# Kernel optimization log

Measured on AMD Instinct MI355X. Metric: run time of the kernel, lower is better.

Reference implementation:

```python
import jax, jax.numpy as jnp
import numpy as np

HIDDEN = 1024
N_HEADS = 16
HEAD_DIM = HIDDEN // N_HEADS
WINDOW = 256
HALF_W = WINDOW // 2  # 128
GLOBAL_TOKENS = (0,)


def setup_inputs() -> dict:
    key = jax.random.key(0)
    ks = jax.random.split(key, 5)
    B, S = 1, 4096
    scale = 0.02
    return {
        "x": jax.random.normal(ks[0], (B, S, HIDDEN), dtype=jnp.float32),
        "Wq": jax.random.normal(ks[1], (HIDDEN, HIDDEN), dtype=jnp.float32) * scale,
        "Wk": jax.random.normal(ks[2], (HIDDEN, HIDDEN), dtype=jnp.float32) * scale,
        "Wv": jax.random.normal(ks[3], (HIDDEN, HIDDEN), dtype=jnp.float32) * scale,
        "Wo": jax.random.normal(ks[4], (HIDDEN, HIDDEN), dtype=jnp.float32) * scale,
    }


def _longformer_mask(seq_len: int) -> jnp.ndarray:
    # sliding window |i-j| <= half_w, plus full rows/cols for global tokens
    idx = jnp.arange(seq_len)
    mask = jnp.abs(idx[:, None] - idx[None, :]) <= HALF_W
    for g in GLOBAL_TOKENS:
        if 0 <= g < seq_len:
            mask = mask.at[g, :].set(True)
            mask = mask.at[:, g].set(True)
    return mask  # [S, S] bool


def reference(x, Wq, Wk, Wv, Wo):
    B, S, H = x.shape
    scale = HEAD_DIM ** -0.5
    # nn.Linear(bias=False): y = x @ W.T ; split heads -> [B, nH, S, hd]
    def proj(W):
        return jnp.einsum('bsh,oh->bso', x, W).reshape(B, S, N_HEADS, HEAD_DIM).transpose(0, 2, 1, 3)
    q, k, v = proj(Wq), proj(Wk), proj(Wv)
    scores = jnp.einsum('bnsd,bntd->bnst', q, k) * scale  # [B, nH, S, S]
    mask = _longformer_mask(S)
    scores = jnp.where(mask[None, None], scores, jnp.float32(-jnp.inf))
    attn = jax.nn.softmax(scores, axis=-1)
    out = jnp.einsum('bnst,bntd->bnsd', attn, v)  # [B, nH, S, hd]
    out = out.transpose(0, 2, 1, 3).reshape(B, S, H)
    return jnp.einsum('bsh,oh->bso', out, Wo)
```

## Files before the change

### kernel.cpp

```cpp
#include <hip/hip_runtime.h>
#include <hip/hip_bf16.h>
#include <stdint.h>

#define S_LEN 4096
#define HID   1024
#define NH    16
#define HD    64
#define HWIN  128

typedef __bf16 bf16x8 __attribute__((ext_vector_type(8)));
typedef float  f32x4  __attribute__((ext_vector_type(4)));
typedef unsigned short u16x8 __attribute__((ext_vector_type(8)));

typedef const __attribute__((address_space(1))) unsigned int* gas_ptr;
typedef __attribute__((address_space(3))) unsigned int* las_ptr;

__device__ __forceinline__ float bf2f(unsigned short u) {
  union { float f; uint32_t i; } w; w.i = ((uint32_t)u) << 16; return w.f;
}
__device__ __forceinline__ unsigned short f2bf(float f) {
  union { float f; uint32_t i; } w; w.f = f;
  uint32_t r = (w.i + 0x7FFFu + ((w.i >> 16) & 1u)) >> 16;
  return (unsigned short)r;
}

__device__ __forceinline__ void gld_lds16(const void* g, void* l) {
  __builtin_amdgcn_global_load_lds((gas_ptr)g, (las_ptr)l, 16, 0, 0);
}

__global__ __launch_bounds__(256) void convert_all(
    const float* __restrict__ x,
    const float* __restrict__ wq, const float* __restrict__ wk,
    const float* __restrict__ wv, const float* __restrict__ wo,
    unsigned short* __restrict__ xb,
    unsigned short* __restrict__ wqb, unsigned short* __restrict__ wkb,
    unsigned short* __restrict__ wvb, unsigned short* __restrict__ wob) {
  const float* in; unsigned short* out; int n4;
  switch (blockIdx.y) {
    case 0:  in = x;  out = xb;  n4 = (S_LEN * HID) / 4; break;
    case 1:  in = wq; out = wqb; n4 = (HID * HID) / 4;   break;
    case 2:  in = wk; out = wkb; n4 = (HID * HID) / 4;   break;
    case 3:  in = wv; out = wvb; n4 = (HID * HID) / 4;   break;
    default: in = wo; out = wob; n4 = (HID * HID) / 4;   break;
  }
  int i = blockIdx.x * 256 + threadIdx.x;
  if (i >= n4) return;
  float4 v = reinterpret_cast<const float4*>(in)[i];
  ushort4 o;
  o.x = f2bf(v.x); o.y = f2bf(v.y); o.z = f2bf(v.z); o.w = f2bf(v.w);
  reinterpret_cast<ushort4*>(out)[i] = o;
}

__device__ __forceinline__ void gemm_body(const unsigned short* __restrict__ A,
                                          const unsigned short* __restrict__ B,
                                          unsigned short* __restrict__ Cb,
                                          float* __restrict__ Cf, int mode) {
  __shared__ __align__(16) unsigned short As[128 * 64];
  __shared__ __align__(16) unsigned short Bs[128 * 64];
  constexpr int K = HID;
  const int tid  = threadIdx.x;
  const int lane = tid & 63;
  const int wave = tid >> 6;
  const int wm = wave >> 1, wn = wave & 1;
  const int m0 = blockIdx.x * 128;
  const int n0 = blockIdx.y * 128;
  const int cl = lane & 15, g = lane >> 4;

  f32x4 acc[4][4];
#pragma unroll
  for (int i = 0; i < 4; i++)
#pragma unroll
    for (int j = 0; j < 4; j++) acc[i][j] = f32x4{0.f, 0.f, 0.f, 0.f};

  const unsigned short* Ap[4];
  const unsigned short* Bp[4];
  int ldso[4];
#pragma unroll
  for (int u = 0; u < 4; u++) {
    int s = tid + u * 256;
    int row = s >> 3, c16 = s & 7;
    int sc = ((c16 ^ (row & 7)) << 3);
    Ap[u] = A + (size_t)(m0 + row) * K + sc;
    Bp[u] = B + (size_t)(n0 + row) * K + sc;
    ldso[u] = s * 8;
  }

  for (int k0 = 0; k0 < K; k0 += 64) {
#pragma unroll
    for (int u = 0; u < 4; u++) {
      gld_lds16(Ap[u] + k0, &As[ldso[u]]);
      gld_lds16(Bp[u] + k0, &Bs[ldso[u]]);
    }
    __syncthreads();
#pragma unroll
    for (int kk = 0; kk < 2; kk++) {
      bf16x8 a[4], b[4];
#pragma unroll
      for (int mi = 0; mi < 4; mi++) {
        int row = wm * 64 + mi * 16 + cl;
        int c16 = (kk * 4 + g) ^ (row & 7);
        a[mi] = *reinterpret_cast<const bf16x8*>(&As[row * 64 + c16 * 8]);
      }
#pragma unroll
      for (int ni = 0; ni < 4; ni++) {
        int row = wn * 64 + ni * 16 + cl;
        int c16 = (kk * 4 + g) ^ (row & 7);
        b[ni] = *reinterpret_cast<const bf16x8*>(&Bs[row * 64 + c16 * 8]);
      }
#pragma unroll
      for (int mi = 0; mi < 4; mi++)
#pragma unroll
        for (int ni = 0; ni < 4; ni++)
          acc[mi][ni] = __builtin_amdgcn_mfma_f32_16x16x32_bf16(a[mi], b[ni], acc[mi][ni], 0, 0, 0);
    }
    __syncthreads();
  }

  const int rl = g * 4;
#pragma unroll
  for (int mi = 0; mi < 4; mi++)
#pragma unroll
    for (int ni = 0; ni < 4; ni++)
#pragma unroll
      for (int i = 0; i < 4; i++) {
        int r = m0 + wm * 64 + mi * 16 + rl + i;
        int c = n0 + wn * 64 + ni * 16 + cl;
        float v = acc[mi][ni][i];
        if (mode == 2)      Cf[(size_t)r * HID + c] = v;
        else if (mode == 1) Cb[(size_t)c * S_LEN + r] = f2bf(v);
        else                Cb[(size_t)r * HID + c] = f2bf(v);
      }
}

__global__ __launch_bounds__(256, 2) void gemm_qkv(
    const unsigned short* __restrict__ xb,
    const unsigned short* __restrict__ wqb, const unsigned short* __restrict__ wkb,
    const unsigned short* __restrict__ wvb,
    unsigned short* __restrict__ Qb, unsigned short* __restrict__ Kb,
    unsigned short* __restrict__ Vt) {
  const unsigned short* B = (blockIdx.z == 0) ? wqb : (blockIdx.z == 1) ? wkb : wvb;
  unsigned short* C       = (blockIdx.z == 0) ? Qb  : (blockIdx.z == 1) ? Kb  : Vt;
  int mode = (blockIdx.z == 2) ? 1 : 0;
  gemm_body(xb, B, C, nullptr, mode);
}

__global__ __launch_bounds__(256, 2) void gemm_proj(
    const unsigned short* __restrict__ Ob, const unsigned short* __restrict__ wob,
    float* __restrict__ out) {
  gemm_body(Ob, wob, nullptr, out, 2);
}

__global__ __launch_bounds__(256) void attn_win(
    const unsigned short* __restrict__ Qb,
    const unsigned short* __restrict__ Kb,
    const unsigned short* __restrict__ Vt,
    unsigned short* __restrict__ Ob) {
  __shared__ __align__(16) unsigned short Kl[2][64 * 64];
  __shared__ __align__(16) unsigned short Vl[2][64 * 64];
  __shared__ __align__(16) unsigned short Ps[4][16 * 64];
  const int L  = (blockIdx.x & 7) * 128 + (blockIdx.x >> 3);
  const int h  = L >> 6;
  const int q0 = (L & 63) * 64;
  const int tid  = threadIdx.x;
  const int lane = tid & 63;
  const int wave = tid >> 6;
  const int qr   = q0 + wave * 16;
  const int cl = lane & 15, g = lane >> 4, rl = g * 4;
  const float SCL = 0.125f * 1.44269504f;

  int kw0 = q0 - 128; if (kw0 < 0) kw0 = 0;
  int kw1 = q0 + 192; if (kw1 > S_LEN) kw1 = S_LEN;
  const int nc = (kw1 - kw0) >> 6;

  const int s0 = tid, s1 = tid + 256;
  const int kr0 = s0 >> 3, kc0 = ((s0 & 7) ^ (kr0 & 7)) << 3;
  const int kr1 = s1 >> 3, kc1 = ((s1 & 7) ^ (kr1 & 7)) << 3;
  const unsigned short* Kbase = Kb + h * HD;
  const unsigned short* Vbase = Vt + (size_t)h * HD * S_LEN;

  auto stage = [&](int kb, int b) {
    gld_lds16(Kbase + (size_t)(kb + kr0) * HID + kc0, &Kl[b][s0 * 8]);
    gld_lds16(Kbase + (size_t)(kb + kr1) * HID + kc1, &Kl[b][s1 * 8]);
    gld_lds16(Vbase + (size_t)kr0 * S_LEN + kb + kc0, &Vl[b][s0 * 8]);
    gld_lds16(Vbase + (size_t)kr1 * S_LEN + kb + kc1, &Vl[b][s1 * 8]);
  };

  stage(kw0, 0);

  bf16x8 qf[2], k0f[2];
  {
    const unsigned short* qb = Qb + (size_t)(qr + cl) * HID + h * HD + g * 8;
    qf[0] = *reinterpret_cast<const bf16x8*>(qb);
    qf[1] = *reinterpret_cast<const bf16x8*>(qb + 32);
    const unsigned short* k0 = Kb + h * HD + g * 8;
    k0f[0] = *reinterpret_cast<const bf16x8*>(k0);
    k0f[1] = *reinterpret_cast<const bf16x8*>(k0 + 32);
  }
  float v0[4];
#pragma unroll
  for (int nt = 0; nt < 4; nt++)
    v0[nt] = bf2f(Vt[(size_t)(h * HD + nt * 16 + cl) * S_LEN]);

  float m_i[4] = {-1e30f, -1e30f, -1e30f, -1e30f};
  float l_i[4] = {0.f, 0.f, 0.f, 0.f};
  f32x4 oacc[4];
#pragma unroll
  for (int nt = 0; nt < 4; nt++) oacc[nt] = f32x4{0.f, 0.f, 0.f, 0.f};

  __syncthreads();

  for (int c = 0; c < nc; c++) {
    const int cur = c & 1;
    const int kb = kw0 + c * 64;
    if (c + 1 < nc) stage(kw0 + (c + 1) * 64, cur ^ 1);

    bf16x8 kf[4][2];
#pragma unroll
    for (int t = 0; t < 4; t++) {
      int R = t * 16 + cl;
      kf[t][0] = *reinterpret_cast<const bf16x8*>(&Kl[cur][R * 64 + ((g ^ (R & 7)) << 3)]);
      kf[t][1] = *reinterpret_cast<const bf16x8*>(&Kl[cur][R * 64 + (((g + 4) ^ (R & 7)) << 3)]);
    }
    f32x4 s4[4];
#pragma unroll
    for (int t = 0; t < 4; t++) {
      s4[t] = f32x4{0.f, 0.f, 0.f, 0.f};
      s4[t] = __builtin_amdgcn_mfma_f32_16x16x32_bf16(qf[0], kf[t][0], s4[t], 0, 0, 0);
      s4[t] = __builtin_amdgcn_mfma_f32_16x16x32_bf16(qf[1], kf[t][1], s4[t], 0, 0, 0);
    }
    float sv[4][4], tm[4];
    if (kb >= qr - 113 && kb <= qr + 65) {
#pragma unroll
      for (int i = 0; i < 4; i++) {
        tm[i] = -1e30f;
#pragma unroll
        for (int t = 0; t < 4; t++) {
          float v = s4[t][i] * SCL;
          sv[t][i] = v;
          tm[i] = fmaxf(tm[i], v);
        }
      }
    } else {
#pragma unroll
      for (int i = 0; i < 4; i++) {
        int row = qr + rl + i;
        tm[i] = -1e30f;
#pragma unroll
        for (int t = 0; t < 4; t++) {
          int col = kb + t * 16 + cl;
          int d = row - col;
          float v = (d <= HWIN && d >= -HWIN) ? s4[t][i] * SCL : -1e30f;
          sv[t][i] = v;
          tm[i] = fmaxf(tm[i], v);
        }
      }
    }
#pragma unroll
    for (int dd = 1; dd < 16; dd <<= 1)
#pragma unroll
      for (int i = 0; i < 4; i++) tm[i] = fmaxf(tm[i], __shfl_xor(tm[i], dd, 16));

    float p[4][4], ps[4];
#pragma unroll
    for (int i = 0; i < 4; i++) {
      float mnew = fmaxf(m_i[i], tm[i]);
      float fac  = exp2f(m_i[i] - mnew);
      m_i[i] = mnew;
      float sum = 0.f;
#pragma unroll
      for (int t = 0; t < 4; t++) { p[t][i] = exp2f(sv[t][i] - mnew); sum += p[t][i]; }
      ps[i] = sum;
      l_i[i] *= fac;
#pragma unroll
      for (int nt = 0; nt < 4; nt++) oacc[nt][i] *= fac;
    }
#pragma unroll
    for (int dd = 1; dd < 16; dd <<= 1)
#pragma unroll
      for (int i = 0; i < 4; i++) ps[i] += __shfl_xor(ps[i], dd, 16);
#pragma unroll
    for (int i = 0; i < 4; i++) l_i[i] += ps[i];

#pragma unroll
    for (int t = 0; t < 4; t++)
#pragma unroll
      for (int i = 0; i < 4; i++) {
        int row = rl + i;
        Ps[wave][row * 64 + ((t * 16 + cl) ^ ((row & 7) << 3))] = f2bf(p[t][i]);
      }
    bf16x8 pf[2];
    pf[0] = *reinterpret_cast<const bf16x8*>(&Ps[wave][cl * 64 + ((g * 8) ^ ((cl & 7) << 3))]);
    pf[1] = *reinterpret_cast<const bf16x8*>(&Ps[wave][cl * 64 + ((32 + g * 8) ^ ((cl & 7) << 3))]);

#pragma unroll
    for (int nt = 0; nt < 4; nt++) {
      int row = nt * 16 + cl;
      bf16x8 vf0 = *reinterpret_cast<const bf16x8*>(&Vl[cur][row * 64 + ((g ^ (row & 7)) << 3)]);
      bf16x8 vf1 = *reinterpret_cast<const bf16x8*>(&Vl[cur][row * 64 + (((g + 4) ^ (row & 7)) << 3)]);
      oacc[nt] = __builtin_amdgcn_mfma_f32_16x16x32_bf16(pf[0], vf0, oacc[nt], 0, 0, 0);
      oacc[nt] = __builtin_amdgcn_mfma_f32_16x16x32_bf16(pf[1], vf1, oacc[nt], 0, 0, 0);
    }

    __syncthreads();
  }

  float part = 0.f;
#pragma unroll
  for (int s = 0; s < 2; s++)
#pragma unroll
    for (int j = 0; j < 8; j++) part += (float)qf[s][j] * (float)k0f[s][j];
  part += __shfl_xor(part, 16);
  part += __shfl_xor(part, 32);
  float s0q = part * SCL;
#pragma unroll
  for (int i = 0; i < 4; i++) {
    float z0 = __shfl(s0q, rl + i, 16);
    int row = qr + rl + i;
    if (row > HWIN) {
      float mnew = fmaxf(m_i[i], z0);
      float fac  = exp2f(m_i[i] - mnew);
      float p0   = exp2f(z0 - mnew);
      l_i[i] = l_i[i] * fac + p0;
#pragma unroll
      for (int nt = 0; nt < 4; nt++)
        oacc[nt][i] = oacc[nt][i] * fac + p0 * v0[nt];
    }
  }

#pragma unroll
  for (int nt = 0; nt < 4; nt++)
#pragma unroll
    for (int i = 0; i < 4; i++)
      Ob[(size_t)(qr + rl + i) * HID + h * HD + nt * 16 + cl] = f2bf(oacc[nt][i] / l_i[i]);
}

__global__ __launch_bounds__(256) void attn_row0_part(
    const unsigned short* __restrict__ Qb,
    const unsigned short* __restrict__ Kb,
    const unsigned short* __restrict__ Vt,
    float* __restrict__ mw, float* __restrict__ lw, float* __restrict__ ow) {
  const int h = blockIdx.y, c = blockIdx.x;
  const int tid = threadIdx.x, lane = tid & 63, wave = tid >> 6;
  const int k = c * 256 + tid;
  __shared__ float qsh[HD];
  __shared__ float ps[256];
  __shared__ float redm[4], redl[4];
  __shared__ float red2[4][HD];
  const float LOG2E = 1.44269504f;

  if (tid < HD) qsh[tid] = bf2f(Qb[h * HD + tid]);
  __syncthreads();

  const unsigned short* kr = Kb + (size_t)k * HID + h * HD;
  float acc = 0.f;
#pragma unroll
  for (int v8 = 0; v8 < 8; v8++) {
    u16x8 kv = *reinterpret_cast<const u16x8*>(kr + v8 * 8);
#pragma unroll
    for (int j = 0; j < 8; j++) acc += qsh[v8 * 8 + j] * bf2f(kv[j]);
  }
  float s = acc * 0.125f;

  float m = s;
#pragma unroll
  for (int d = 1; d < 64; d <<= 1) m = fmaxf(m, __shfl_xor(m, d, 64));
  if (lane == 0) redm[wave] = m;
  __syncthreads();
  float m_c = fmaxf(fmaxf(redm[0], redm[1]), fmaxf(redm[2], redm[3]));

  float p = exp2f((s - m_c) * LOG2E);
  ps[tid] = p;
  float l = p;
#pragma unroll
  for (int d = 1; d < 64; d <<= 1) l += __shfl_xor(l, d, 64);
  if (lane == 0) redl[wave] = l;
  __syncthreads();
  float l_c = redl[0] + redl[1] + redl[2] + redl[3];

  const int d = tid & 63, grp = tid >> 6;
  const unsigned short* vrow = Vt + (size_t)(h * HD + d) * S_LEN + c * 256 + grp * 64;
  float a2 = 0.f;
#pragma unroll
  for (int v8 = 0; v8 < 8; v8++) {
    u16x8 vv = *reinterpret_cast<const u16x8*>(vrow + v8 * 8);
#pragma unroll
    for (int j = 0; j < 8; j++) a2 += ps[grp * 64 + v8 * 8 + j] * bf2f(vv[j]);
  }
  red2[grp][d] = a2;
  __syncthreads();
  if (tid < HD) {
    float o = red2[0][tid] + red2[1][tid] + red2[2][tid] + red2[3][tid];
    ow[(size_t)(h * 16 + c) * HD + tid] = o;
  }
  if (tid == 0) { mw[h * 16 + c] = m_c; lw[h * 16 + c] = l_c; }
}

__global__ __launch_bounds__(64) void attn_row0_fin(
    const float* __restrict__ mw, const float* __restrict__ lw,
    const float* __restrict__ ow, unsigned short* __restrict__ Ob) {
  const int h = blockIdx.x, d = threadIdx.x;
  const float LOG2E = 1.44269504f;
  float m_g = -1e30f;
#pragma unroll
  for (int c = 0; c < 16; c++) m_g = fmaxf(m_g, mw[h * 16 + c]);
  float lsum = 0.f, osum = 0.f;
#pragma unroll
  for (int c = 0; c < 16; c++) {
    float w = exp2f((mw[h * 16 + c] - m_g) * LOG2E);
    lsum += lw[h * 16 + c] * w;
    osum += ow[(size_t)(h * 16 + c) * HD + d] * w;
  }
  Ob[h * HD + d] = f2bf(osum / lsum);
}

extern "C" void kernel_launch(void* const* d_in, const int* in_sizes, int n_in,
                              void* d_out, int out_size, void* d_ws, size_t ws_size,
                              hipStream_t stream) {
  const float* x  = (const float*)d_in[0];
  const float* wq = (const float*)d_in[1];
  const float* wk = (const float*)d_in[2];
  const float* wv = (const float*)d_in[3];
  const float* wo = (const float*)d_in[4];
  float* out = (float*)d_out;
  char* ws = (char*)d_ws;
  const size_t MB = 1024ull * 1024ull;
  unsigned short* xb  = (unsigned short*)(ws + 0 * MB);
  unsigned short* wqb = (unsigned short*)(ws + 8 * MB);
  unsigned short* wkb = (unsigned short*)(ws + 10 * MB);
  unsigned short* wvb = (unsigned short*)(ws + 12 * MB);
  unsigned short* wob = (unsigned short*)(ws + 14 * MB);
  unsigned short* Qb  = (unsigned short*)(ws + 16 * MB);
  unsigned short* Kb  = (unsigned short*)(ws + 24 * MB);
  unsigned short* Vt  = (unsigned short*)(ws + 32 * MB);
  unsigned short* Ob  = (unsigned short*)(ws + 40 * MB);
  float* mw = (float*)(ws + 48 * MB);
  float* lw = (float*)(ws + 48 * MB + 4096);
  float* ow = (float*)(ws + 48 * MB + 8192);

  dim3 blk(256);
  convert_all<<<dim3((S_LEN * HID / 4 + 255) / 256, 5), blk, 0, stream>>>(
      x, wq, wk, wv, wo, xb, wqb, wkb, wvb, wob);
  gemm_qkv<<<dim3(S_LEN / 128, HID / 128, 3), blk, 0, stream>>>(
      xb, wqb, wkb, wvb, Qb, Kb, Vt);
  attn_win<<<dim3(1024), blk, 0, stream>>>(Qb, Kb, Vt, Ob);
  attn_row0_part<<<dim3(16, NH), blk, 0, stream>>>(Qb, Kb, Vt, mw, lw, ow);
  attn_row0_fin<<<dim3(NH), dim3(64), 0, stream>>>(mw, lw, ow, Ob);
  gemm_proj<<<dim3(S_LEN / 128, HID / 128), blk, 0, stream>>>(Ob, wob, out);
}
```

Baseline: 104.1 us.

## Rewrite QKV GEMM with 256x256 tiles and double-buffered LDS prefetch

The QKV projection GEMM becomes a dedicated 512-thread kernel. Each block computes a 256x256 tile with 8 waves, and the A and B LDS buffers are double-buffered. The next K-tile's global-to-LDS loads are issued in pieces while MFMAs run on the current buffer, with explicit barriers, waitcnts and s_setprio around the MFMA bursts. This aims to hide load latency and raise MFMA density, but it cuts the grid to 192 blocks, fewer than the CU count, and the large LDS footprint (about 128KB) limits each CU to one block.

```diff
diff --git a/kernel.cpp b/kernel.cpp
--- a/kernel.cpp
+++ b/kernel.cpp
@@ -51,10 +51,115 @@
   reinterpret_cast<ushort4*>(out)[i] = o;
 }
 
-__device__ __forceinline__ void gemm_body(const unsigned short* __restrict__ A,
-                                          const unsigned short* __restrict__ B,
-                                          unsigned short* __restrict__ Cb,
-                                          float* __restrict__ Cf, int mode) {
+__global__ __launch_bounds__(512, 2) void gemm_qkv(
+    const unsigned short* __restrict__ xb,
+    const unsigned short* __restrict__ wqb, const unsigned short* __restrict__ wkb,
+    const unsigned short* __restrict__ wvb,
+    unsigned short* __restrict__ Qb, unsigned short* __restrict__ Kb,
+    unsigned short* __restrict__ Vt) {
+  __shared__ __align__(16) unsigned short As[2][2][128 * 64];
+  __shared__ __align__(16) unsigned short Bs[2][2][128 * 64];
+  const unsigned short* Bw = (blockIdx.z == 0) ? wqb : (blockIdx.z == 1) ? wkb : wvb;
+  unsigned short* C        = (blockIdx.z == 0) ? Qb  : (blockIdx.z == 1) ? Kb  : Vt;
+  const int mode = (blockIdx.z == 2) ? 1 : 0;
+  constexpr int K = HID;
+  constexpr int NT = K / 64;
+  const int tid  = threadIdx.x;
+  const int lane = tid & 63;
+  const int wid  = tid >> 6;
+  const int wm = wid >> 2, wn = wid & 3;
+  const int m0 = blockIdx.x * 256;
+  const int n0 = blockIdx.y * 256;
+  const int cl = lane & 15, g = lane >> 4;
+
+  f32x4 acc[8][4];
+#pragma unroll
+  for (int i = 0; i < 8; i++)
+#pragma unroll
+    for (int j = 0; j < 4; j++) acc[i][j] = f32x4{0.f, 0.f, 0.f, 0.f};
+
+  const int s0 = tid, s1 = tid + 512;
+  const int r0 = s0 >> 3, c0 = ((s0 & 7) ^ (r0 & 7)) << 3;
+  const int r1 = s1 >> 3, c1 = ((s1 & 7) ^ (r1 & 7)) << 3;
+
+  auto stageA = [&](int t, int half, int b) {
+    const unsigned short* src = xb + (size_t)(m0 + half * 128) * K + t * 64;
+    gld_lds16(src + (size_t)r0 * K + c0, &As[b][half][s0 * 8]);
+    gld_lds16(src + (size_t)r1 * K + c1, &As[b][half][s1 * 8]);
+  };
+  auto stageB = [&](int t, int half, int b) {
+    const unsigned short* src = Bw + (size_t)(n0 + half * 128) * K + t * 64;
+    gld_lds16(src + (size_t)r0 * K + c0, &Bs[b][half][s0 * 8]);
+    gld_lds16(src + (size_t)r1 * K + c1, &Bs[b][half][s1 * 8]);
+  };
+
+  stageA(0, 0, 0); stageA(0, 1, 0); stageB(0, 0, 0); stageB(0, 1, 0);
+
+  const int brow0 = (wn & 1) * 64;
+  for (int t = 0; t < NT; ++t) {
+    const int cur = t & 1, nxt = cur ^ 1;
+    asm volatile("s_waitcnt vmcnt(0)" ::: "memory");
+    __builtin_amdgcn_s_barrier();
+    __builtin_amdgcn_sched_barrier(0);
+    const unsigned short* Ab = &As[cur][wm][0];
+    const unsigned short* Bb = &Bs[cur][wn >> 1][0];
+    bf16x8 a[4], b[4];
+#pragma unroll
+    for (int q = 0; q < 4; ++q) {
+      const int kk = q >> 1, mih = q & 1;
+      if (t + 1 < NT) {
+        if (q == 0)      stageA(t + 1, 0, nxt);
+        else if (q == 1) stageA(t + 1, 1, nxt);
+        else if (q == 2) stageB(t + 1, 0, nxt);
+        else             stageB(t + 1, 1, nxt);
+      }
+      if (mih == 0) {
+#pragma unroll
+        for (int ni = 0; ni < 4; ni++) {
+          int row = brow0 + ni * 16 + cl;
+          b[ni] = *reinterpret_cast<const bf16x8*>(
+              &Bb[row * 64 + (((kk * 4 + g) ^ (row & 7)) << 3)]);
+        }
+      }
+#pragma unroll
+      for (int mi = 0; mi < 4; mi++) {
+        int row = (mih * 4 + mi) * 16 + cl;
+        a[mi] = *reinterpret_cast<const bf16x8*>(
+            &Ab[row * 64 + (((kk * 4 + g) ^ (row & 7)) << 3)]);
+      }
+      __builtin_amdgcn_s_barrier();
+      asm volatile("s_waitcnt lgkmcnt(0)" ::: "memory");
+      __builtin_amdgcn_sched_barrier(0);
+      __builtin_amdgcn_s_setprio(1);
+#pragma unroll
+      for (int mi = 0; mi < 4; mi++)
+#pragma unroll
+        for (int ni = 0; ni < 4; ni++)
+          acc[mih * 4 + mi][ni] =
+              __builtin_amdgcn_mfma_f32_16x16x32_bf16(a[mi], b[ni], acc[mih * 4 + mi][ni], 0, 0, 0);
+      __builtin_amdgcn_s_setprio(0);
+      __builtin_amdgcn_s_barrier();
+    }
+  }
+
+  const int rl = g * 4;
+#pragma unroll
+  for (int mi = 0; mi < 8; mi++)
+#pragma unroll
+    for (int ni = 0; ni < 4; ni++)
+#pragma unroll
+      for (int i = 0; i < 4; i++) {
+        int r = m0 + wm * 128 + mi * 16 + rl + i;
+        int c = n0 + wn * 64 + ni * 16 + cl;
+        float v = acc[mi][ni][i];
+        if (mode == 1) C[(size_t)c * S_LEN + r] = f2bf(v);
+        else           C[(size_t)r * HID + c] = f2bf(v);
+      }
+}
+
+__global__ __launch_bounds__(256, 2) void gemm_proj(
+    const unsigned short* __restrict__ Ob, const unsigned short* __restrict__ wob,
+    float* __restrict__ out) {
   __shared__ __align__(16) unsigned short As[128 * 64];
   __shared__ __align__(16) unsigned short Bs[128 * 64];
   constexpr int K = HID;
@@ -80,8 +185,8 @@
     int s = tid + u * 256;
     int row = s >> 3, c16 = s & 7;
     int sc = ((c16 ^ (row & 7)) << 3);
-    Ap[u] = A + (size_t)(m0 + row) * K + sc;
-    Bp[u] = B + (size_t)(n0 + row) * K + sc;
+    Ap[u] = Ob + (size_t)(m0 + row) * K + sc;
+    Bp[u] = wob + (size_t)(n0 + row) * K + sc;
     ldso[u] = s * 8;
   }
 
@@ -125,29 +230,8 @@
       for (int i = 0; i < 4; i++) {
         int r = m0 + wm * 64 + mi * 16 + rl + i;
         int c = n0 + wn * 64 + ni * 16 + cl;
-        float v = acc[mi][ni][i];
-        if (mode == 2)      Cf[(size_t)r * HID + c] = v;
-        else if (mode == 1) Cb[(size_t)c * S_LEN + r] = f2bf(v);
-        else                Cb[(size_t)r * HID + c] = f2bf(v);
-      }
-}
-
-__global__ __launch_bounds__(256, 2) void gemm_qkv(
-    const unsigned short* __restrict__ xb,
-    const unsigned short* __restrict__ wqb, const unsigned short* __restrict__ wkb,
-    const unsigned short* __restrict__ wvb,
-    unsigned short* __restrict__ Qb, unsigned short* __restrict__ Kb,
-    unsigned short* __restrict__ Vt) {
-  const unsigned short* B = (blockIdx.z == 0) ? wqb : (blockIdx.z == 1) ? wkb : wvb;
-  unsigned short* C       = (blockIdx.z == 0) ? Qb  : (blockIdx.z == 1) ? Kb  : Vt;
-  int mode = (blockIdx.z == 2) ? 1 : 0;
-  gemm_body(xb, B, C, nullptr, mode);
-}
-
-__global__ __launch_bounds__(256, 2) void gemm_proj(
-    const unsigned short* __restrict__ Ob, const unsigned short* __restrict__ wob,
-    float* __restrict__ out) {
-  gemm_body(Ob, wob, nullptr, out, 2);
+        out[(size_t)r * HID + c] = acc[mi][ni][i];
+      }
 }
 
 __global__ __launch_bounds__(256) void attn_win(
@@ -440,7 +524,7 @@
   dim3 blk(256);
   convert_all<<<dim3((S_LEN * HID / 4 + 255) / 256, 5), blk, 0, stream>>>(
       x, wq, wk, wv, wo, xb, wqb, wkb, wvb, wob);
-  gemm_qkv<<<dim3(S_LEN / 128, HID / 128, 3), blk, 0, stream>>>(
+  gemm_qkv<<<dim3(S_LEN / 256, HID / 256, 3), dim3(512), 0, stream>>>(
       xb, wqb, wkb, wvb, Qb, Kb, Vt);
   attn_win<<<dim3(1024), blk, 0, stream>>>(Qb, Kb, Vt, Ob);
   attn_row0_part<<<dim3(16, NH), blk, 0, stream>>>(Qb, Kb, Vt, mw, lw, ow);
```

Result: slower. 148.7 us (+42.8%).
